# Kernel tuning notes

Hardware: AMD Instinct MI355X
Metric: run time of the kernel (lower is better)

## Reference

```python
import jax, jax.numpy as jnp
import numpy as np

GROUPS = 32
EPS = 1e-6


def group_norm(x, gamma, beta):
    b, c, h, w = x.shape
    xg = x.reshape(b, GROUPS, c // GROUPS, h, w)
    mu = xg.mean(axis=(2, 3, 4), keepdims=True)
    var = xg.var(axis=(2, 3, 4), keepdims=True)
    xn = ((xg - mu) * jax.lax.rsqrt(var + EPS)).reshape(b, c, h, w)
    return xn * gamma[None, :, None, None] + beta[None, :, None, None]


def conv1x1(x, w, b):
    # x: (b,c_in,h,w), w: (c_out,c_in), b: (c_out,)
    return jnp.einsum('oc,bchw->bohw', w, x) + b[None, :, None, None]


def setup_inputs() -> dict:
    key = jax.random.key(0)
    ks = jax.random.split(key, 10)
    c = 512
    scale = 1.0 / np.sqrt(c)
    inp = jax.random.normal(ks[0], (16, c, 32, 32), dtype=jnp.float32)
    return {
        'inp': inp,
        'gamma': jnp.ones((c,), jnp.float32),
        'beta': jnp.zeros((c,), jnp.float32),
        'Wq': jax.random.normal(ks[1], (c, c), jnp.float32) * scale,
        'bq': jnp.zeros((c,), jnp.float32),
        'Wk': jax.random.normal(ks[2], (c, c), jnp.float32) * scale,
        'bk': jnp.zeros((c,), jnp.float32),
        'Wv': jax.random.normal(ks[3], (c, c), jnp.float32) * scale,
        'bv': jnp.zeros((c,), jnp.float32),
        'Wo': jax.random.normal(ks[4], (c, c), jnp.float32) * scale,
        'bo': jnp.zeros((c,), jnp.float32),
    }


def reference(inp, gamma, beta, Wq, bq, Wk, bk, Wv, bv, Wo, bo):
    b, c, h, w = inp.shape
    x = group_norm(inp, gamma, beta)
    Q = conv1x1(x, Wq, bq).reshape(b, c, h * w)  # (b,c,n)
    K = conv1x1(x, Wk, bk).reshape(b, c, h * w)  # (b,c,m)
    V = conv1x1(x, Wv, bv).reshape(b, c, h * w)  # (b,c,m)
    # attn[b,n,m] = sum_c Q[b,c,n] * K[b,c,m], scaled then softmax over m
    attn = jnp.einsum('bcn,bcm->bnm', Q, K) / jnp.sqrt(jnp.float32(c))
    attn = jax.nn.softmax(attn, axis=2)
    # A[b,c,n] = sum_m V[b,c,m] * attn[b,n,m]  (== bmm(V, attn^T))
    A = jnp.einsum('bcm,bnm->bcn', V, attn).reshape(b, c, h, w)
    A = conv1x1(A, Wo, bo)
    return inp + A
```

## Files before the change

kernel.cpp:

```cpp
#include <hip/hip_runtime.h>

typedef unsigned short UST;
typedef __attribute__((ext_vector_type(8))) short bf16x8;
typedef __attribute__((ext_vector_type(8))) unsigned short us8;
typedef __attribute__((ext_vector_type(4))) float f32x4;

__device__ __forceinline__ UST f2bf(float f) {
  union { float f; unsigned int u; } x; x.f = f;
  unsigned int r = x.u + 0x7fffu + ((x.u >> 16) & 1u);
  return (UST)(r >> 16);
}
__device__ __forceinline__ float bf2f(UST h) {
  union { unsigned int u; float f; } x; x.u = ((unsigned int)h) << 16;
  return x.f;
}

__device__ __forceinline__ void sync_lds() {
  asm volatile("s_waitcnt lgkmcnt(0)\n\ts_barrier" ::: "memory");
}
__device__ __forceinline__ void barrier_nowait() {
  asm volatile("s_barrier" ::: "memory");
}

__global__ __launch_bounds__(256) void conv_w(
    const float4* __restrict__ wq, const float4* __restrict__ wk,
    const float4* __restrict__ wv, const float4* __restrict__ wo,
    ushort4* __restrict__ oqkv, ushort4* __restrict__ owo,
    const float4* __restrict__ bq4, const float4* __restrict__ bk4,
    const float4* __restrict__ bv4, float4* __restrict__ bqkv4) {
  int i = blockIdx.x * 256 + threadIdx.x;
  float4 v;
  v = wq[i]; oqkv[i]          = make_ushort4(f2bf(v.x), f2bf(v.y), f2bf(v.z), f2bf(v.w));
  v = wk[i]; oqkv[i + 65536]  = make_ushort4(f2bf(v.x), f2bf(v.y), f2bf(v.z), f2bf(v.w));
  v = wv[i]; oqkv[i + 131072] = make_ushort4(f2bf(v.x), f2bf(v.y), f2bf(v.z), f2bf(v.w));
  v = wo[i]; owo[i]           = make_ushort4(f2bf(v.x), f2bf(v.y), f2bf(v.z), f2bf(v.w));
  if (blockIdx.x < 2) {
    int t = blockIdx.x * 256 + threadIdx.x;
    if (t < 384) bqkv4[t] = (t < 128) ? bq4[t] : (t < 256 ? bk4[t - 128] : bv4[t - 256]);
  }
}

__global__ __launch_bounds__(256) void gn_fused(
    const float* __restrict__ inp, const float* __restrict__ gamma,
    const float* __restrict__ beta, UST* __restrict__ Xnt) {
  const int g = blockIdx.x & 31, b = blockIdx.x >> 5;
  const int tid = threadIdx.x;
  const float* base = inp + ((size_t)b * 32 + g) * 16384;
  const float4* p4 = (const float4*)base;
  float s = 0.f, ss = 0.f;
#pragma unroll
  for (int i = 0; i < 16; i++) {
    float4 t = p4[tid + i * 256];
    s += t.x + t.y + t.z + t.w;
    ss += t.x * t.x + t.y * t.y + t.z * t.z + t.w * t.w;
  }
  for (int o = 32; o >= 1; o >>= 1) { s += __shfl_xor(s, o); ss += __shfl_xor(ss, o); }
  __shared__ float red[8];
  __shared__ float mu_s, rstd_s;
  const int w = tid >> 6;
  if ((tid & 63) == 0) { red[w * 2] = s; red[w * 2 + 1] = ss; }
  __syncthreads();
  if (tid == 0) {
    float S1 = red[0] + red[2] + red[4] + red[6];
    float S2 = red[1] + red[3] + red[5] + red[7];
    float mu = S1 * (1.f / 16384.f);
    float var = S2 * (1.f / 16384.f) - mu * mu;
    mu_s = mu; rstd_s = rsqrtf(var + 1e-6f);
  }
  __syncthreads();
  const float mu = mu_s, rstd = rstd_s;
#pragma unroll
  for (int cc = 0; cc < 2; cc++) {
    const int ccg = g * 2 + cc;
    float sc[8], sh[8];
#pragma unroll
    for (int j = 0; j < 8; j++) {
      int ch = ccg * 8 + j;
      sc[j] = gamma[ch] * rstd;
      sh[j] = beta[ch] - mu * sc[j];
    }
#pragma unroll
    for (int i = 0; i < 4; i++) {
      const int n = tid + i * 256;
      us8 v;
#pragma unroll
      for (int j = 0; j < 8; j++) {
        float x = inp[((size_t)b * 512 + ccg * 8 + j) * 1024 + n];
        v[j] = f2bf(x * sc[j] + sh[j]);
      }
      *(us8*)(Xnt + (size_t)b * 524288 + (size_t)ccg * 8192 + (size_t)n * 8) = v;
    }
  }
}

__global__ __launch_bounds__(256) void softmax_k(const UST* __restrict__ S,
                                                 UST* __restrict__ P) {
  const int w = threadIdx.x >> 6, lane = threadIdx.x & 63;
  const size_t row = (size_t)blockIdx.x * 4 + w;
  const us8* Sr = (const us8*)(S + row * 1024);
  us8 a = Sr[lane], b = Sr[64 + lane];
  float v[16];
#pragma unroll
  for (int j = 0; j < 8; j++) { v[j] = bf2f(a[j]); v[8 + j] = bf2f(b[j]); }
  float m = v[0];
#pragma unroll
  for (int i = 1; i < 16; i++) m = fmaxf(m, v[i]);
#pragma unroll
  for (int o = 32; o >= 1; o >>= 1) m = fmaxf(m, __shfl_xor(m, o));
  float s = 0.f;
#pragma unroll
  for (int i = 0; i < 16; i++) { v[i] = __expf(v[i] - m); s += v[i]; }
#pragma unroll
  for (int o = 32; o >= 1; o >>= 1) s += __shfl_xor(s, o);
  const float rs = 1.f / s;
  us8* Pr = (us8*)(P + row * 1024);
  us8 oa, ob;
#pragma unroll
  for (int j = 0; j < 8; j++) { oa[j] = f2bf(v[j] * rs); ob[j] = f2bf(v[8 + j] * rs); }
  Pr[lane] = oa; Pr[64 + lane] = ob;
}

template <int EPI>
__global__ __launch_bounds__(256, 2) void gemm_bt(
    const UST* __restrict__ A, const UST* __restrict__ B, void* __restrict__ C,
    const float* __restrict__ bias, const float* __restrict__ extra, float scale,
    int K, int ldc,
    int rsA, int csA, int ssA, int rsB, int csB, int ssB,
    long zA, long zB, long zC) {
  __shared__ __align__(16) UST buf[10240];
  UST* lA = buf;
  UST* lB = buf + 5120;

  const int tid = threadIdx.x;
  const int z = blockIdx.z;
  const int m0 = blockIdx.y * 128;
  const int n0 = blockIdx.x * 128;
  const UST* Ab = A + (long)z * zA;
  const UST* Bb = B + (long)z * zB;

  const int w = tid >> 6, lane = tid & 63;
  const int quad = lane >> 4, l16 = lane & 15;
  const int wm = w >> 1, wn = w & 1;

  f32x4 acc[4][4];
#pragma unroll
  for (int i = 0; i < 4; i++)
#pragma unroll
    for (int j = 0; j < 4; j++) acc[i][j] = f32x4{0.f, 0.f, 0.f, 0.f};

  const int rowa = tid >> 2;
  const int kchunk = tid & 3;
  const UST* gA = Ab + (size_t)(m0 + rowa) * rsA + (size_t)kchunk * csA;
  const UST* gB = Bb + (size_t)(n0 + rowa) * rsB + (size_t)kchunk * csB;
  const size_t a64 = (size_t)64 * rsA, b64 = (size_t)64 * rsB;
  UST* wA = lA + rowa * 40 + kchunk * 8;
  UST* wB = lB + rowa * 40 + kchunk * 8;

  us8 pa0 = *(const us8*)gA, pa1 = *(const us8*)(gA + a64);
  us8 pb0 = *(const us8*)gB, pb1 = *(const us8*)(gB + b64);

  const int nk = K >> 5;
  for (int k = 0; k < nk; ++k) {
    us8 na0, na1, nb0, nb1;
    if (k + 1 < nk) {
      gA += ssA; gB += ssB;
      na0 = *(const us8*)gA; na1 = *(const us8*)(gA + a64);
      nb0 = *(const us8*)gB; nb1 = *(const us8*)(gB + b64);
    }
    if (k) barrier_nowait();
    *(us8*)wA = pa0; *(us8*)(wA + 2560) = pa1;
    *(us8*)wB = pb0; *(us8*)(wB + 2560) = pb1;
    sync_lds();
    bf16x8 af[4], bfr[4];
#pragma unroll
    for (int i = 0; i < 4; i++)
      af[i] = *(const bf16x8*)(lA + (wm * 64 + i * 16 + l16) * 40 + quad * 8);
#pragma unroll
    for (int j = 0; j < 4; j++)
      bfr[j] = *(const bf16x8*)(lB + (wn * 64 + j * 16 + l16) * 40 + quad * 8);
#pragma unroll
    for (int i = 0; i < 4; i++)
#pragma unroll
      for (int j = 0; j < 4; j++)
        acc[i][j] = __builtin_amdgcn_mfma_f32_16x16x32_bf16(af[i], bfr[j], acc[i][j], 0, 0, 0);
    pa0 = na0; pa1 = na1; pb0 = nb0; pb1 = nb1;
  }

  barrier_nowait();

  if constexpr (EPI == 4) {
    float* fbuf = (float*)buf;
    float* Cb = (float*)C + (long)z * zC;
    const float* Eb = extra + (long)z * zC;
#pragma unroll
    for (int p = 0; p < 4; ++p) {
      if (p) barrier_nowait();
      if (wm == (p >> 1)) {
#pragma unroll
        for (int ii = 0; ii < 2; ii++) {
          const int i = (p & 1) * 2 + ii;
#pragma unroll
          for (int j = 0; j < 4; j++)
#pragma unroll
            for (int r = 0; r < 4; r++)
              fbuf[(ii * 16 + quad * 4 + r) * 132 + wn * 64 + j * 16 + l16] = acc[i][j][r];
        }
      }
      sync_lds();
#pragma unroll
      for (int it = 0; it < 4; ++it) {
        int q = tid + it * 256;
        int row = q >> 5, colc = q & 31;
        int gr = m0 + p * 32 + row;
        size_t off = (size_t)gr * ldc + n0 + colc * 4;
        float4 v = *(float4*)&fbuf[row * 132 + colc * 4];
        float4 e = *(const float4*)&Eb[off];
        float bb = bias[gr];
        v.x += bb + e.x; v.y += bb + e.y; v.z += bb + e.z; v.w += bb + e.w;
        *(float4*)&Cb[off] = v;
      }
    }
  } else {
    const bool vreg = (EPI == 6) && (n0 >= 1024);
    if (!vreg) {
      UST* Cb = (UST*)C + (long)z * zC;
#pragma unroll
      for (int h = 0; h < 2; ++h) {
        if (h) barrier_nowait();
        if (wm == h) {
#pragma unroll
          for (int i = 0; i < 4; i++)
#pragma unroll
            for (int j = 0; j < 4; j++) {
              float bc = 0.f;
              if constexpr (EPI == 6) bc = bias[n0 + wn * 64 + j * 16 + l16];
#pragma unroll
              for (int r = 0; r < 4; r++) {
                float v = acc[i][j][r] + bc;
                if constexpr (EPI == 5) v *= scale;
                buf[(i * 16 + quad * 4 + r) * 136 + wn * 64 + j * 16 + l16] = f2bf(v);
              }
            }
        }
        sync_lds();
#pragma unroll
        for (int it = 0; it < 4; ++it) {
          int q = tid + it * 256;
          int row = q >> 4, colc = q & 15;
          us8 v = *(us8*)&buf[row * 136 + colc * 8];
          *(us8*)&Cb[(size_t)(m0 + h * 64 + row) * ldc + n0 + colc * 8] = v;
        }
      }
    } else {
      UST* Vb = (UST*)extra + (long)z * 524288;
#pragma unroll
      for (int h = 0; h < 2; ++h) {
        if (h) barrier_nowait();
        if (wn == h) {
#pragma unroll
          for (int i = 0; i < 4; i++)
#pragma unroll
            for (int j = 0; j < 4; j++) {
              const float bc = bias[n0 + wn * 64 + j * 16 + l16];
#pragma unroll
              for (int r = 0; r < 4; r++) {
                float v = acc[i][j][r] + bc;
                buf[(j * 16 + l16) * 136 + wm * 64 + i * 16 + quad * 4 + r] = f2bf(v);
              }
            }
        }
        sync_lds();
#pragma unroll
        for (int it = 0; it < 4; ++it) {
          int q = tid + it * 256;
          int c = q >> 4, mc = q & 15;
          us8 v = *(us8*)&buf[c * 136 + mc * 8];
          *(us8*)&Vb[(size_t)(n0 - 1024 + h * 64 + c) * 1024 + m0 + mc * 8] = v;
        }
      }
    }
  }
}

extern "C" void kernel_launch(void* const* d_in, const int* in_sizes, int n_in,
                              void* d_out, int out_size, void* d_ws, size_t ws_size,
                              hipStream_t stream) {
  const float* inp   = (const float*)d_in[0];
  const float* gamma = (const float*)d_in[1];
  const float* beta  = (const float*)d_in[2];
  const float* Wq    = (const float*)d_in[3];
  const float* bq    = (const float*)d_in[4];
  const float* Wk    = (const float*)d_in[5];
  const float* bk    = (const float*)d_in[6];
  const float* Wv    = (const float*)d_in[7];
  const float* bv    = (const float*)d_in[8];
  const float* Wo    = (const float*)d_in[9];
  const float* bo    = (const float*)d_in[10];
  float* out = (float*)d_out;
  char* ws = (char*)d_ws;

  UST*   Xnt   = (UST*)(ws);
  UST*   QKt   = (UST*)(ws + ((size_t)16 << 20));
  UST*   V     = (UST*)(ws + ((size_t)48 << 20));
  UST*   S     = (UST*)(ws + ((size_t)64 << 20));
  float* bqkv  = (float*)(ws + ((size_t)96 << 20));
  UST*   Wqkvb = (UST*)(ws + ((size_t)96 << 20) + 8192);
  UST*   Wob   = Wqkvb + 786432;
  UST*   P     = QKt;
  UST*   At    = Xnt;

  conv_w<<<256, 256, 0, stream>>>(
      (const float4*)Wq, (const float4*)Wk, (const float4*)Wv, (const float4*)Wo,
      (ushort4*)Wqkvb, (ushort4*)Wob,
      (const float4*)bq, (const float4*)bk, (const float4*)bv, (float4*)bqkv);
  gn_fused<<<512, 256, 0, stream>>>(inp, gamma, beta, Xnt);

  gemm_bt<6><<<dim3(12, 8, 16), 256, 0, stream>>>(
      Xnt, Wqkvb, QKt, bqkv, (const float*)V, 1.f,
      512, 1024, 8, 8192, 32768, 512, 8, 32, 524288, 0, 1048576);
  gemm_bt<5><<<dim3(8, 8, 16), 256, 0, stream>>>(
      QKt, QKt + 512, S, nullptr, nullptr, 0.04419417382415922f,
      512, 1024, 1024, 8, 32, 1024, 8, 32, 1048576, 1048576, 1048576);
  softmax_k<<<4096, 256, 0, stream>>>(S, P);
  gemm_bt<3><<<dim3(4, 8, 16), 256, 0, stream>>>(
      P, V, At, nullptr, nullptr, 1.f,
      1024, 512, 1024, 8, 32, 1024, 8, 32, 1048576, 524288, 524288);
  gemm_bt<4><<<dim3(8, 4, 16), 256, 0, stream>>>(
      Wob, At, out, bo, inp, 1.f,
      512, 1024, 512, 8, 32, 512, 8, 32, 0, 524288, 524288);
}
```

Before: 238.5 us.

## Double-buffer A tile in LDS and load B fragments directly from global

Restructures the GEMM main loop: the A tile is double-buffered in LDS so only one barrier per k-step is needed and the next tile is written while the current one is consumed. The B operand bypasses LDS entirely; each wave loads its MFMA fragments straight from global memory with two-deep register prefetch. This removes half the LDS traffic and one barrier per iteration, at the cost of more registers (which may hurt 2-blocks-per-CU occupancy) and less coalesced global loads for B, since each lane reads 16 bytes at a row stride.

New measurement: 317.6 us. +33.2%, slower.

```diff
diff --git a/kernel.cpp b/kernel.cpp
--- a/kernel.cpp
+++ b/kernel.cpp
@@ -128,8 +128,8 @@
     int rsA, int csA, int ssA, int rsB, int csB, int ssB,
     long zA, long zB, long zC) {
   __shared__ __align__(16) UST buf[10240];
-  UST* lA = buf;
-  UST* lB = buf + 5120;
+  UST* buf0 = buf;
+  UST* buf1 = buf + 5120;
 
   const int tid = threadIdx.x;
   const int z = blockIdx.z;
@@ -151,42 +151,57 @@
   const int rowa = tid >> 2;
   const int kchunk = tid & 3;
   const UST* gA = Ab + (size_t)(m0 + rowa) * rsA + (size_t)kchunk * csA;
-  const UST* gB = Bb + (size_t)(n0 + rowa) * rsB + (size_t)kchunk * csB;
-  const size_t a64 = (size_t)64 * rsA, b64 = (size_t)64 * rsB;
-  UST* wA = lA + rowa * 40 + kchunk * 8;
-  UST* wB = lB + rowa * 40 + kchunk * 8;
-
-  us8 pa0 = *(const us8*)gA, pa1 = *(const us8*)(gA + a64);
-  us8 pb0 = *(const us8*)gB, pb1 = *(const us8*)(gB + b64);
+  const size_t a64 = (size_t)64 * rsA;
+  const int lw = rowa * 40 + kchunk * 8;
+
+  const UST* gBf = Bb + (size_t)(n0 + wn * 64 + l16) * rsB + (size_t)quad * csB;
+  const size_t b16 = (size_t)16 * rsB;
 
   const int nk = K >> 5;
+
+  bf16x8 bcur[4], bnxt[4];
+#pragma unroll
+  for (int j = 0; j < 4; j++) bcur[j] = *(const bf16x8*)(gBf + j * b16);
+  {
+    const UST* g1 = gBf + (size_t)(nk > 1 ? 1 : 0) * ssB;
+#pragma unroll
+    for (int j = 0; j < 4; j++) bnxt[j] = *(const bf16x8*)(g1 + j * b16);
+  }
+
+  us8 pa0 = *(const us8*)gA;
+  us8 pa1 = *(const us8*)(gA + a64);
+  *(us8*)(buf0 + lw) = pa0;
+  *(us8*)(buf0 + lw + 2560) = pa1;
+  if (nk > 1) { gA += ssA; pa0 = *(const us8*)gA; pa1 = *(const us8*)(gA + a64); }
+  sync_lds();
+
   for (int k = 0; k < nk; ++k) {
-    us8 na0, na1, nb0, nb1;
+    UST* cur = (k & 1) ? buf1 : buf0;
+    UST* nxt = (k & 1) ? buf0 : buf1;
+    bf16x8 af[4];
+#pragma unroll
+    for (int i = 0; i < 4; i++)
+      af[i] = *(const bf16x8*)(cur + (wm * 64 + i * 16 + l16) * 40 + quad * 8);
+    bf16x8 b2[4];
+    if (k + 2 < nk) {
+      const UST* g2 = gBf + (size_t)(k + 2) * ssB;
+#pragma unroll
+      for (int j = 0; j < 4; j++) b2[j] = *(const bf16x8*)(g2 + j * b16);
+    }
     if (k + 1 < nk) {
-      gA += ssA; gB += ssB;
-      na0 = *(const us8*)gA; na1 = *(const us8*)(gA + a64);
-      nb0 = *(const us8*)gB; nb1 = *(const us8*)(gB + b64);
-    }
-    if (k) barrier_nowait();
-    *(us8*)wA = pa0; *(us8*)(wA + 2560) = pa1;
-    *(us8*)wB = pb0; *(us8*)(wB + 2560) = pb1;
+      *(us8*)(nxt + lw) = pa0;
+      *(us8*)(nxt + lw + 2560) = pa1;
+      if (k + 2 < nk) { gA += ssA; pa0 = *(const us8*)gA; pa1 = *(const us8*)(gA + a64); }
+    }
+#pragma unroll
+    for (int i = 0; i < 4; i++)
+#pragma unroll
+      for (int j = 0; j < 4; j++)
+        acc[i][j] = __builtin_amdgcn_mfma_f32_16x16x32_bf16(af[i], bcur[j], acc[i][j], 0, 0, 0);
     sync_lds();
-    bf16x8 af[4], bfr[4];
-#pragma unroll
-    for (int i = 0; i < 4; i++)
-      af[i] = *(const bf16x8*)(lA + (wm * 64 + i * 16 + l16) * 40 + quad * 8);
-#pragma unroll
-    for (int j = 0; j < 4; j++)
-      bfr[j] = *(const bf16x8*)(lB + (wn * 64 + j * 16 + l16) * 40 + quad * 8);
-#pragma unroll
-    for (int i = 0; i < 4; i++)
-#pragma unroll
-      for (int j = 0; j < 4; j++)
-        acc[i][j] = __builtin_amdgcn_mfma_f32_16x16x32_bf16(af[i], bfr[j], acc[i][j], 0, 0, 0);
-    pa0 = na0; pa1 = na1; pb0 = nb0; pb1 = nb1;
-  }
-
-  barrier_nowait();
+#pragma unroll
+    for (int j = 0; j < 4; j++) { bcur[j] = bnxt[j]; bnxt[j] = b2[j]; }
+  }
 
   if constexpr (EPI == 4) {
     float* fbuf = (float*)buf;
```
